# Performance work log

Hardware: AMD Instinct MI355X
Metric: run time of the kernel (lower is better)

## Reference

```python
import jax, jax.numpy as jnp
import numpy as np

B, D, O = 512, 512, 512  # batch, indim, outdim

def setup_inputs() -> dict:
    key = jax.random.key(0)
    k1, k2, k3 = jax.random.split(key, 3)
    x = jax.random.normal(k1, (B, D), dtype=jnp.float32)
    mu_weight = jax.random.normal(k2, (O, D), dtype=jnp.float32) / np.sqrt(D)
    # inverse diagonal covariance entries (positive in spirit; uniform fill)
    inv_diag_C_weight = jax.random.uniform(k3, (O, D), dtype=jnp.float32)
    return {"x": x, "mu_weight": mu_weight, "inv_diag_C_weight": inv_diag_C_weight}

def reference(x, mu_weight, inv_diag_C_weight):
    # Original: logits = -(x-mu) @ diag(invC) @ (x-mu)^T per (batch, class) pair.
    # Diagonal structure => elementwise squared diff weighted by invC, summed over D.
    diff = x[:, None, :] - mu_weight[None, :, :]            # [B, O, D]
    logits = -jnp.einsum('bod,od->bo', diff * diff, inv_diag_C_weight)
    return logits                                            # [B, O]
```

## Files before the change

### kernel.cpp

```cpp
#include <hip/hip_runtime.h>

#define B_DIM 512
#define D_DIM 512
#define O_DIM 512
#define KSPLIT 8
#define DCHUNK 64


__global__ __launch_bounds__(256, 2)
void gda_main(const float* __restrict__ x,
              const float* __restrict__ mu,
              const float* __restrict__ ic,
              float* __restrict__ ws) {
    __shared__ float4 lds_x4[64 * 16];
    __shared__ float4 lds_ab4[64 * 16 * 2];
    __shared__ float  lds_cp[64 * 16];
    __shared__ float  lds_c[64];

    const int tid = threadIdx.x;
    const int bid = blockIdx.x;
    const int bb = bid & 7, ob = (bid >> 3) & 7, ks = bid >> 6;
    const int b0 = bb * 64, o0 = ob * 64, d0 = ks * DCHUNK;

    const int g   = tid & 15;
    const int row = tid >> 4;
#pragma unroll
    for (int i = 0; i < 4; ++i) {
        const int r = row + 16 * i;
        const int sw = g ^ (r & 7);
        const float4 xv = *(const float4*)&x [(b0 + r) * D_DIM + d0 + g * 4];
        lds_x4[r * 16 + sw] = xv;
        const float4 m4 = *(const float4*)&mu[(o0 + r) * D_DIM + d0 + g * 4];
        const float4 c4 = *(const float4*)&ic[(o0 + r) * D_DIM + d0 + g * 4];
        float4 a4, b4;
        a4.x = -c4.x;            a4.y = -c4.y;
        a4.z = -c4.z;            a4.w = -c4.w;
        b4.x = 2.0f * m4.x * c4.x; b4.y = 2.0f * m4.y * c4.y;
        b4.z = 2.0f * m4.z * c4.z; b4.w = 2.0f * m4.w * c4.w;
        lds_ab4[(r * 16 + sw) * 2 + 0] = a4;
        lds_ab4[(r * 16 + sw) * 2 + 1] = b4;
        lds_cp[r * 16 + g] = m4.x * m4.x * c4.x + m4.y * m4.y * c4.y
                           + m4.z * m4.z * c4.z + m4.w * m4.w * c4.w;
    }
    __syncthreads();

    if (tid < 64) {
        float s = 0.0f;
#pragma unroll
        for (int q = 0; q < 16; ++q) s += lds_cp[tid * 16 + q];
        lds_c[tid] = -s;
    }

    const int w    = tid >> 6;
    const int lane = tid & 63;
    const int cb   = lane >> 3;
    const int r8   = lane & 7;
    const int wb   = (w & 1) * 32, wo = (w >> 1) * 32;

    float acc[16];
#pragma unroll
    for (int q = 0; q < 16; ++q) acc[q] = 0.0f;

#pragma unroll
    for (int gg = 0; gg < 16; ++gg) {
        float4 xr[4], xs[4];
#pragma unroll
        for (int k = 0; k < 4; ++k) {
            xr[k] = lds_x4[(wb + cb + 8 * k) * 16 + (gg ^ cb)];
            xs[k].x = xr[k].x * xr[k].x;
            xs[k].y = xr[k].y * xr[k].y;
            xs[k].z = xr[k].z * xr[k].z;
            xs[k].w = xr[k].w * xr[k].w;
        }
#pragma unroll
        for (int j = 0; j < 4; ++j) {
            const int oo = wo + r8 + 8 * j;
            const float4 a4 = lds_ab4[(oo * 16 + (gg ^ r8)) * 2 + 0];
            const float4 b4 = lds_ab4[(oo * 16 + (gg ^ r8)) * 2 + 1];
#pragma unroll
            for (int k = 0; k < 4; ++k) {
                float t = acc[k * 4 + j];
                t = fmaf(a4.x, xs[k].x, t);  t = fmaf(b4.x, xr[k].x, t);
                t = fmaf(a4.y, xs[k].y, t);  t = fmaf(b4.y, xr[k].y, t);
                t = fmaf(a4.z, xs[k].z, t);  t = fmaf(b4.z, xr[k].z, t);
                t = fmaf(a4.w, xs[k].w, t);  t = fmaf(b4.w, xr[k].w, t);
                acc[k * 4 + j] = t;
            }
        }
    }
    __syncthreads();

    float* wsb = (float*)ws + (size_t)bid * 4096;
#pragma unroll
    for (int j = 0; j < 4; ++j) {
        const float cc = lds_c[wo + r8 + 8 * j];
#pragma unroll
        for (int k = 0; k < 4; ++k)
            wsb[(wb + cb + 8 * k) * 64 + (wo + r8 + 8 * j)] = acc[k * 4 + j] + cc;
    }
}

__global__ __launch_bounds__(256, 4)
void gda_reduce(const float* __restrict__ ws, float* __restrict__ out) {
    const int t0 = blockIdx.x * 1024 + threadIdx.x;
#pragma unroll
    for (int p = 0; p < 4; ++p) {
        const int flat = t0 + p * 256;
        const int b = flat >> 9, o = flat & 511;
        const int bb = b >> 6, bl = b & 63, ob = o >> 6, ol = o & 63;
        const float* base = ws + ((ob * 8 + bb) * 4096 + bl * 64 + ol);
        float s = 0.0f;
#pragma unroll
        for (int k = 0; k < KSPLIT; ++k) s += base[k * (64 * 4096)];
        out[flat] = s;
    }
}

extern "C" void kernel_launch(void* const* d_in, const int* in_sizes, int n_in,
                              void* d_out, int out_size, void* d_ws, size_t ws_size,
                              hipStream_t stream) {
    const float* x  = (const float*)d_in[0];
    const float* mu = (const float*)d_in[1];
    const float* ic = (const float*)d_in[2];
    float* ws  = (float*)d_ws;
    float* out = (float*)d_out;

    gda_main  <<<dim3(512), dim3(256), 0, stream>>>(x, mu, ic, ws);
    gda_reduce<<<dim3(256), dim3(256), 0, stream>>>(ws, out);
}
```

Measured before the change: 74.35 us.

## Replace FP32 split-K FMA kernel with single bf16 MFMA GEMM kernel

Expands the squared-difference sum into a GEMM whose K dimension is doubled ([x^2, x] times [-c, 2mc]). It converts operands to bf16 and computes the tiles with 16x16x32 MFMA instructions. The split-K workspace and separate reduction kernel are dropped, so each 32x32 output tile loops over all of D in one block and writes the output directly. This removes a launch and the workspace round-trip, at the cost of bf16 rounding error, notably on the x^2 and 2mc terms that partially cancel.

Result: faster. 64.14 us (-13.7%).

```diff
diff --git a/kernel.cpp b/kernel.cpp
--- a/kernel.cpp
+++ b/kernel.cpp
@@ -1,118 +1,124 @@
 #include <hip/hip_runtime.h>
+#include <hip/hip_bf16.h>
 
 #define B_DIM 512
 #define D_DIM 512
 #define O_DIM 512
-#define KSPLIT 8
-#define DCHUNK 64
+#define DCH   128
+#define NCH   (D_DIM/DCH)
 
 
-__global__ __launch_bounds__(256, 2)
-void gda_main(const float* __restrict__ x,
+typedef __attribute__((ext_vector_type(8))) short short8;
+typedef __attribute__((ext_vector_type(4))) float f32x4;
+
+__device__ __forceinline__ short f2bf(float f) {
+    union { __hip_bfloat16 h; unsigned short u; } cv;
+    cv.h = __float2bfloat16(f);
+    return (short)cv.u;
+}
+
+__global__ __launch_bounds__(256)
+void gda_mfma(const float* __restrict__ x,
               const float* __restrict__ mu,
               const float* __restrict__ ic,
-              float* __restrict__ ws) {
-    __shared__ float4 lds_x4[64 * 16];
-    __shared__ float4 lds_ab4[64 * 16 * 2];
-    __shared__ float  lds_cp[64 * 16];
-    __shared__ float  lds_c[64];
+              float* __restrict__ out)
+{
+    __shared__ unsigned short A_lds[32 * 256];
+    __shared__ unsigned short B_lds[32 * 256];
+    __shared__ float          c_part[32 * 8];
+    __shared__ float          c_o[32];
 
     const int tid = threadIdx.x;
     const int bid = blockIdx.x;
-    const int bb = bid & 7, ob = (bid >> 3) & 7, ks = bid >> 6;
-    const int b0 = bb * 64, o0 = ob * 64, d0 = ks * DCHUNK;
+    const int b0 = (bid & 15) * 32;
+    const int o0 = (bid >> 4) * 32;
 
-    const int g   = tid & 15;
-    const int row = tid >> 4;
+    const int srow = tid >> 3;
+    const int su   = tid & 7;
+
+    const int w    = tid >> 6;
+    const int lane = tid & 63;
+    const int wr   = w >> 1;
+    const int wc   = w & 1;
+    const int fcol = lane & 15;
+    const int fk   = lane >> 4;
+
+    const int rowA = wr * 16 + fcol;
+    const int rowB = wc * 16 + fcol;
+    const int swA7 = rowA & 7;
+    const int swB7 = rowB & 7;
+
+    float creg = 0.0f;
+    f32x4 acc = {0.0f, 0.0f, 0.0f, 0.0f};
+
+    for (int ch = 0; ch < NCH; ++ch) {
+        const int d0 = ch * DCH;
+
 #pragma unroll
-    for (int i = 0; i < 4; ++i) {
-        const int r = row + 16 * i;
-        const int sw = g ^ (r & 7);
-        const float4 xv = *(const float4*)&x [(b0 + r) * D_DIM + d0 + g * 4];
-        lds_x4[r * 16 + sw] = xv;
-        const float4 m4 = *(const float4*)&mu[(o0 + r) * D_DIM + d0 + g * 4];
-        const float4 c4 = *(const float4*)&ic[(o0 + r) * D_DIM + d0 + g * 4];
-        float4 a4, b4;
-        a4.x = -c4.x;            a4.y = -c4.y;
-        a4.z = -c4.z;            a4.w = -c4.w;
-        b4.x = 2.0f * m4.x * c4.x; b4.y = 2.0f * m4.y * c4.y;
-        b4.z = 2.0f * m4.z * c4.z; b4.w = 2.0f * m4.w * c4.w;
-        lds_ab4[(r * 16 + sw) * 2 + 0] = a4;
-        lds_ab4[(r * 16 + sw) * 2 + 1] = b4;
-        lds_cp[r * 16 + g] = m4.x * m4.x * c4.x + m4.y * m4.y * c4.y
-                           + m4.z * m4.z * c4.z + m4.w * m4.w * c4.w;
+        for (int half = 0; half < 2; ++half) {
+            const int uu  = su + half * 8;
+            const int swz = uu ^ (srow & 7);
+            const int dd  = d0 + uu * 8;
+
+            {
+                const float4 p = *(const float4*)&x[(b0 + srow) * D_DIM + dd];
+                const float4 q = *(const float4*)&x[(b0 + srow) * D_DIM + dd + 4];
+                const float v[8] = {p.x, p.y, p.z, p.w, q.x, q.y, q.z, q.w};
+                short8 s2, s1;
+#pragma unroll
+                for (int e = 0; e < 8; ++e) {
+                    s2[e] = f2bf(v[e] * v[e]);
+                    s1[e] = f2bf(v[e]);
+                }
+                *(short8*)&A_lds[(srow * 32 + swz) * 8]      = s2;
+                *(short8*)&A_lds[(srow * 32 + 16 + swz) * 8] = s1;
+            }
+            {
+                const int rbase = (o0 + srow) * D_DIM + dd;
+                const float4 m0 = *(const float4*)&mu[rbase];
+                const float4 m1 = *(const float4*)&mu[rbase + 4];
+                const float4 c0 = *(const float4*)&ic[rbase];
+                const float4 c1 = *(const float4*)&ic[rbase + 4];
+                const float mv[8] = {m0.x, m0.y, m0.z, m0.w, m1.x, m1.y, m1.z, m1.w};
+                const float cf[8] = {c0.x, c0.y, c0.z, c0.w, c1.x, c1.y, c1.z, c1.w};
+                short8 sa, sb;
+#pragma unroll
+                for (int e = 0; e < 8; ++e) {
+                    sa[e] = f2bf(-cf[e]);
+                    sb[e] = f2bf(2.0f * mv[e] * cf[e]);
+                    creg  = fmaf(mv[e] * mv[e], cf[e], creg);
+                }
+                *(short8*)&B_lds[(srow * 32 + swz) * 8]      = sa;
+                *(short8*)&B_lds[(srow * 32 + 16 + swz) * 8] = sb;
+            }
+        }
+        __syncthreads();
+
+#pragma unroll
+        for (int ks = 0; ks < 8; ++ks) {
+            const int g  = ks * 4 + fk;
+            const short8 av = *(const short8*)&A_lds[(rowA * 32 + (g ^ swA7)) * 8];
+            const short8 bv = *(const short8*)&B_lds[(rowB * 32 + (g ^ swB7)) * 8];
+            acc = __builtin_amdgcn_mfma_f32_16x16x32_bf16(av, bv, acc, 0, 0, 0);
+        }
+        __syncthreads();
+    }
+
+    c_part[srow * 8 + su] = creg;
+    __syncthreads();
+    if (tid < 32) {
+        float s = 0.0f;
+#pragma unroll
+        for (int q = 0; q < 8; ++q) s += c_part[tid * 8 + q];
+        c_o[tid] = s;
     }
     __syncthreads();
 
-    if (tid < 64) {
-        float s = 0.0f;
 #pragma unroll
-        for (int q = 0; q < 16; ++q) s += lds_cp[tid * 16 + q];
-        lds_c[tid] = -s;
-    }
-
-    const int w    = tid >> 6;
-    const int lane = tid & 63;
-    const int cb   = lane >> 3;
-    const int r8   = lane & 7;
-    const int wb   = (w & 1) * 32, wo = (w >> 1) * 32;
-
-    float acc[16];
-#pragma unroll
-    for (int q = 0; q < 16; ++q) acc[q] = 0.0f;
-
-#pragma unroll
-    for (int gg = 0; gg < 16; ++gg) {
-        float4 xr[4], xs[4];
-#pragma unroll
-        for (int k = 0; k < 4; ++k) {
-            xr[k] = lds_x4[(wb + cb + 8 * k) * 16 + (gg ^ cb)];
-            xs[k].x = xr[k].x * xr[k].x;
-            xs[k].y = xr[k].y * xr[k].y;
-            xs[k].z = xr[k].z * xr[k].z;
-            xs[k].w = xr[k].w * xr[k].w;
-        }
-#pragma unroll
-        for (int j = 0; j < 4; ++j) {
-            const int oo = wo + r8 + 8 * j;
-            const float4 a4 = lds_ab4[(oo * 16 + (gg ^ r8)) * 2 + 0];
-            const float4 b4 = lds_ab4[(oo * 16 + (gg ^ r8)) * 2 + 1];
-#pragma unroll
-            for (int k = 0; k < 4; ++k) {
-                float t = acc[k * 4 + j];
-                t = fmaf(a4.x, xs[k].x, t);  t = fmaf(b4.x, xr[k].x, t);
-                t = fmaf(a4.y, xs[k].y, t);  t = fmaf(b4.y, xr[k].y, t);
-                t = fmaf(a4.z, xs[k].z, t);  t = fmaf(b4.z, xr[k].z, t);
-                t = fmaf(a4.w, xs[k].w, t);  t = fmaf(b4.w, xr[k].w, t);
-                acc[k * 4 + j] = t;
-            }
-        }
-    }
-    __syncthreads();
-
-    float* wsb = (float*)ws + (size_t)bid * 4096;
-#pragma unroll
-    for (int j = 0; j < 4; ++j) {
-        const float cc = lds_c[wo + r8 + 8 * j];
-#pragma unroll
-        for (int k = 0; k < 4; ++k)
-            wsb[(wb + cb + 8 * k) * 64 + (wo + r8 + 8 * j)] = acc[k * 4 + j] + cc;
-    }
-}
-
-__global__ __launch_bounds__(256, 4)
-void gda_reduce(const float* __restrict__ ws, float* __restrict__ out) {
-    const int t0 = blockIdx.x * 1024 + threadIdx.x;
-#pragma unroll
-    for (int p = 0; p < 4; ++p) {
-        const int flat = t0 + p * 256;
-        const int b = flat >> 9, o = flat & 511;
-        const int bb = b >> 6, bl = b & 63, ob = o >> 6, ol = o & 63;
-        const float* base = ws + ((ob * 8 + bb) * 4096 + bl * 64 + ol);
-        float s = 0.0f;
-#pragma unroll
-        for (int k = 0; k < KSPLIT; ++k) s += base[k * (64 * 4096)];
-        out[flat] = s;
+    for (int r = 0; r < 4; ++r) {
+        const int row = wr * 16 + fk * 4 + r;
+        const int col = wc * 16 + fcol;
+        out[(b0 + row) * O_DIM + o0 + col] = acc[r] - c_o[col];
     }
 }
 
@@ -122,9 +128,7 @@
     const float* x  = (const float*)d_in[0];
     const float* mu = (const float*)d_in[1];
     const float* ic = (const float*)d_in[2];
-    float* ws  = (float*)d_ws;
     float* out = (float*)d_out;
 
-    gda_main  <<<dim3(512), dim3(256), 0, stream>>>(x, mu, ic, ws);
-    gda_reduce<<<dim3(256), dim3(256), 0, stream>>>(ws, out);
+    gda_mfma<<<dim3(256), dim3(256), 0, stream>>>(x, mu, ic, out);
 }
```
